# Kernel tuning notes

Measured on AMD Instinct MI355X. Metric: run time of the kernel, lower is better.

Reference implementation:

```python
import jax, jax.numpy as jnp
import numpy as np

H, KV, HD = 32, 4, 64
REP = H // KV
MAX_POS = 2048


def setup_inputs() -> dict:
    key = jax.random.key(0)
    ks = jax.random.split(key, 6)
    B, S, D = 2, 1024, 2048
    x = jax.random.normal(ks[0], (B, S, D), dtype=jnp.float32)
    wq = jax.random.normal(ks[1], (D, H * HD), dtype=jnp.float32) * 0.02
    wk = jax.random.normal(ks[2], (D, KV * HD), dtype=jnp.float32) * 0.02
    wv = jax.random.normal(ks[3], (D, KV * HD), dtype=jnp.float32) * 0.02
    wo = jax.random.normal(ks[4], (H * HD, D), dtype=jnp.float32) * 0.02
    # RoPE tables: [max_pos, head_dim//2]
    inv_freq = 1.0 / (10000.0 ** (np.arange(0, HD, 2, dtype=np.float32) / HD))
    angles = np.arange(MAX_POS, dtype=np.float32)[:, None] * inv_freq[None, :]
    cos = jnp.asarray(np.cos(angles), dtype=jnp.float32)
    sin = jnp.asarray(np.sin(angles), dtype=jnp.float32)
    # causal additive mask [S, S]
    row = jnp.arange(S)[:, None]
    col = jnp.arange(S)[None, :]
    mask = jnp.where(col <= row, 0.0, -1e9).astype(jnp.float32)
    return {"x": x, "wq": wq, "wk": wk, "wv": wv, "wo": wo,
            "cos": cos, "sin": sin, "mask": mask, "pos": 0}


def _rotate(t, c, s):
    # t: [B,S,Hx,HD]; c,s: [1,S,1,HD//2]
    half = t.shape[-1] // 2
    t1, t2 = t[..., :half], t[..., half:]
    return jnp.concatenate([t1 * c - t2 * s, t2 * c + t1 * s], axis=-1)


def reference(x, wq, wk, wv, wo, cos, sin, mask, pos):
    B, S, D = x.shape
    q = (x @ wq).reshape(B, S, H, HD)
    k = (x @ wk).reshape(B, S, KV, HD)
    v = (x @ wv).reshape(B, S, KV, HD)
    c = cos[pos:pos + S][None, :, None, :]
    s = sin[pos:pos + S][None, :, None, :]
    q = _rotate(q, c, s)
    k = _rotate(k, c, s)
    # prefill: cache[:, 0:S] == fresh k,v, kv_len == S
    # native GQA broadcast: group q heads by kv head instead of repeating k/v
    qg = q.reshape(B, S, KV, REP, HD)
    scores = jnp.einsum('bqkrd,bskd->bkrqs', qg, k) / jnp.sqrt(jnp.float32(HD))
    scores = scores + mask  # mask broadcasts over [B,KV,REP,S,S]
    attn = jax.nn.softmax(scores, axis=-1)
    out = jnp.einsum('bkrqs,bskd->bqkrd', attn, v).reshape(B, S, H * HD)
    return out @ wo
```

## Files before the change

kernel.cpp:

```cpp
#include <hip/hip_runtime.h>

#define B_ 2
#define S_ 1024
#define D_ 2048
#define H_ 32
#define KV_ 4
#define HD_ 64
#define NQKV 2560
#define KVB 64

typedef __attribute__((ext_vector_type(8))) short bf16x8;
typedef __attribute__((ext_vector_type(4))) float f32x4;
typedef __attribute__((ext_vector_type(16))) float f32x16;

__device__ __forceinline__ unsigned short f2bf(float f) {
  unsigned int u = __float_as_uint(f);
  u = (u + 0x7fffu + ((u >> 16) & 1u)) >> 16;
  return (unsigned short)u;
}
__device__ __forceinline__ unsigned int cvt_pk_bf16(float a, float b) {
  unsigned int r;
  asm("v_cvt_pk_bf16_f32 %0, %1, %2" : "=v"(r) : "v"(a), "v"(b));
  return r;
}
__device__ __forceinline__ float exp2f_fast(float x) {
  return __builtin_amdgcn_exp2f(x);
}

#define GLOAD_LDS(gp, lp) \
  __builtin_amdgcn_global_load_lds((const __attribute__((address_space(1))) void*)(gp), \
                                   (__attribute__((address_space(3))) void*)(lp), 16, 0, 0)

__global__ __launch_bounds__(256) void k_convert(const float* __restrict__ src,
                                                 unsigned short* __restrict__ dst, int n4) {
  int i = blockIdx.x * 256 + threadIdx.x;
  if (i >= n4) return;
  float4 v = ((const float4*)src)[i];
  ushort4 o;
  o.x = f2bf(v.x); o.y = f2bf(v.y); o.z = f2bf(v.z); o.w = f2bf(v.w);
  ((ushort4*)dst)[i] = o;
}

__global__ __launch_bounds__(256) void k_transpose4(const float* __restrict__ wq,
                                                    const float* __restrict__ wk,
                                                    const float* __restrict__ wv,
                                                    const float* __restrict__ wo,
                                                    unsigned short* __restrict__ wft,
                                                    unsigned short* __restrict__ wot) {
  __shared__ float tile[32][33];
  const int z = blockIdx.z;
  const float* src;
  unsigned short* dst;
  int N, roff;
  if (z == 0)      { src = wq; dst = wft; N = 2048; roff = 0; }
  else if (z == 1) { src = wk; dst = wft; N = 256;  roff = 2048; }
  else if (z == 2) { src = wv; dst = wft; N = 256;  roff = 2304; }
  else             { src = wo; dst = wot; N = 2048; roff = 0; }
  int n0 = blockIdx.x * 32, k0 = blockIdx.y * 32;
  if (n0 >= N) return;
  int tx = threadIdx.x & 31, ty = threadIdx.x >> 5;
  #pragma unroll
  for (int i = 0; i < 4; ++i)
    tile[ty + 8 * i][tx] = src[(size_t)(k0 + ty + 8 * i) * N + (n0 + tx)];
  __syncthreads();
  #pragma unroll
  for (int i = 0; i < 4; ++i)
    dst[(size_t)(roff + n0 + ty + 8 * i) * D_ + (k0 + tx)] = f2bf(tile[tx][ty + 8 * i]);
}

template <int BM, int BN, int MODE>
__global__ __launch_bounds__(256) void k_gemm(const unsigned short* __restrict__ A,
                                              const unsigned short* __restrict__ Bt,
                                              float* __restrict__ C,
                                              const float* __restrict__ cosT,
                                              const float* __restrict__ sinT,
                                              const int* __restrict__ posp,
                                              unsigned short* __restrict__ q_r,
                                              unsigned short* __restrict__ k_r,
                                              unsigned short* __restrict__ v_t,
                                              int M, int N, int K) {
  constexpr int MR = BM / 32;
  constexpr int NR = BN / 32;
  __shared__ alignas(16) unsigned short As[BM * 64];
  __shared__ alignas(16) unsigned short Bs[BN * 64];
  const int tid = threadIdx.x;
  const int wid = tid >> 6, lane = tid & 63;
  const int lo = lane & 15, hi = lane >> 4;
  const int m0 = blockIdx.y * BM, n0 = blockIdx.x * BN;
  const int wr = wid >> 1, wc = wid & 1;
  f32x4 acc[MR][NR] = {};

  const int nkt = K >> 6;
  for (int kt = 0; kt < nkt; ++kt) {
    __syncthreads();
    #pragma unroll
    for (int u = tid; u < BM * 8; u += 256) {
      int row = u >> 3, ch = u & 7, chs = ch ^ (row & 7);
      GLOAD_LDS(A + (size_t)(m0 + row) * K + kt * 64 + chs * 8, As + u * 8);
    }
    #pragma unroll
    for (int u = tid; u < BN * 8; u += 256) {
      int row = u >> 3, ch = u & 7, chs = ch ^ (row & 7);
      GLOAD_LDS(Bt + (size_t)(n0 + row) * K + kt * 64 + chs * 8, Bs + u * 8);
    }
    __syncthreads();
    #pragma unroll
    for (int ks = 0; ks < 2; ++ks) {
      const int chs = (ks * 4 + hi) ^ (lo & 7);
      bf16x8 a[MR], b[NR];
      #pragma unroll
      for (int m = 0; m < MR; ++m) {
        int row = wr * (BM / 2) + m * 16 + lo;
        a[m] = *(const bf16x8*)(As + row * 64 + chs * 8);
      }
      #pragma unroll
      for (int n = 0; n < NR; ++n) {
        int row = wc * (BN / 2) + n * 16 + lo;
        b[n] = *(const bf16x8*)(Bs + row * 64 + chs * 8);
      }
      #pragma unroll
      for (int m = 0; m < MR; ++m)
        #pragma unroll
        for (int n = 0; n < NR; ++n)
          acc[m][n] = __builtin_amdgcn_mfma_f32_16x16x32_bf16(a[m], b[n], acc[m][n], 0, 0, 0);
    }
  }

  if (MODE == 0) {
    const int cr = hi * 4;
    #pragma unroll
    for (int m = 0; m < MR; ++m)
      #pragma unroll
      for (int n = 0; n < NR; ++n) {
        int col = n0 + wc * (BN / 2) + n * 16 + lo;
        int rowb = m0 + wr * (BM / 2) + m * 16 + cr;
        #pragma unroll
        for (int r = 0; r < 4; ++r)
          C[(size_t)(rowb + r) * N + col] = acc[m][n][r];
      }
  } else {
    const int col0 = n0 + wc * (BN / 2);
    const int pos = posp[0];
    const float qsc = 0.125f * 1.44269504f;
    if (col0 < 2048) {
      const int h = col0 >> 6;
      #pragma unroll
      for (int m = 0; m < MR; ++m)
        #pragma unroll
        for (int r = 0; r < 4; ++r) {
          int row = m0 + wr * (BM / 2) + m * 16 + hi * 4 + r;
          int s = row & (S_ - 1), b = row >> 10;
          unsigned short* base = q_r + ((size_t)(b * H_ + h) * S_ + s) * HD_;
          #pragma unroll
          for (int np = 0; np < 2; ++np) {
            int i = np * 16 + lo;
            float t1 = acc[m][np][r], t2 = acc[m][np + 2][r];
            float c = cosT[(size_t)(pos + s) * 32 + i];
            float sn = sinT[(size_t)(pos + s) * 32 + i];
            base[i] = f2bf((t1 * c - t2 * sn) * qsc);
            base[i + 32] = f2bf((t2 * c + t1 * sn) * qsc);
          }
        }
    } else if (col0 < 2304) {
      const int g = (col0 - 2048) >> 6;
      #pragma unroll
      for (int m = 0; m < MR; ++m)
        #pragma unroll
        for (int r = 0; r < 4; ++r) {
          int row = m0 + wr * (BM / 2) + m * 16 + hi * 4 + r;
          int s = row & (S_ - 1), b = row >> 10;
          unsigned short* base = k_r + ((size_t)(b * KV_ + g) * S_ + s) * HD_;
          #pragma unroll
          for (int np = 0; np < 2; ++np) {
            int i = np * 16 + lo;
            float t1 = acc[m][np][r], t2 = acc[m][np + 2][r];
            float c = cosT[(size_t)(pos + s) * 32 + i];
            float sn = sinT[(size_t)(pos + s) * 32 + i];
            base[i] = f2bf(t1 * c - t2 * sn);
            base[i + 32] = f2bf(t2 * c + t1 * sn);
          }
        }
    } else {
      const int g = (col0 - 2304) >> 6;
      #pragma unroll
      for (int m = 0; m < MR; ++m) {
        int row0 = m0 + wr * (BM / 2) + m * 16 + hi * 4;
        int s0 = row0 & (S_ - 1), b = row0 >> 10;
        #pragma unroll
        for (int n = 0; n < NR; ++n) {
          int d = n * 16 + lo;
          ushort4 o;
          o.x = f2bf(acc[m][n][0]);
          o.y = f2bf(acc[m][n][1]);
          o.z = f2bf(acc[m][n][2]);
          o.w = f2bf(acc[m][n][3]);
          *(ushort4*)(v_t + ((size_t)(b * KV_ + g) * HD_ + d) * S_ + s0) = o;
        }
      }
    }
  }
}

__global__ __launch_bounds__(128) void k_attn(const unsigned short* __restrict__ qr,
                                              const unsigned short* __restrict__ kr,
                                              const unsigned short* __restrict__ vt,
                                              unsigned short* __restrict__ ao) {
  __shared__ alignas(16) unsigned short k_lds[2 * KVB * HD_];
  __shared__ alignas(16) unsigned short v_lds[2 * HD_ * KVB];
  const int tid = threadIdx.x;
  const int wid = tid >> 6, lane = tid & 63;
  const int l31 = lane & 31, hi5 = lane >> 5;
  const int bh = blockIdx.x;
  const int h = bh >> 1, b = bh & 1, g = h >> 3;
  const int qt = 15 - (int)blockIdx.y;
  const int nch = qt + 1;
  const int q_abs = qt * 64 + wid * 32 + l31;

  const unsigned short* qrow = qr + ((size_t)(b * H_ + h) * S_ + q_abs) * HD_;
  bf16x8 qf[4];
  #pragma unroll
  for (int ks = 0; ks < 4; ++ks)
    qf[ks] = *(const bf16x8*)(qrow + ks * 16 + hi5 * 8);

  const unsigned short* kbase = kr + (size_t)(b * KV_ + g) * S_ * HD_;
  const unsigned short* vbase = vt + (size_t)(b * KV_ + g) * HD_ * S_;

  const unsigned short* kg[4];
  const unsigned short* vg[4];
  int ldo[4];
  #pragma unroll
  for (int ii = 0; ii < 4; ++ii) {
    int uu = ii * 128 + tid;
    int r = uu >> 3, ch = uu & 7, chs = ch ^ (r & 7);
    kg[ii] = kbase + r * HD_ + chs * 8;
    vg[ii] = vbase + (size_t)r * S_ + chs * 8;
    ldo[ii] = uu * 8;
  }
  int chs8[4];
  #pragma unroll
  for (int ks = 0; ks < 4; ++ks) chs8[ks] = ((ks * 2 + hi5) ^ (l31 & 7)) * 8;
  const int krow = l31 * 64;

  f32x16 oacc[2] = {};
  float mrun = -1e30f, ls = 0.f;
  int buf = 0;

  auto stage = [&](int c, int bi) {
    #pragma unroll
    for (int ii = 0; ii < 4; ++ii)
      GLOAD_LDS(kg[ii] + (size_t)c * (KVB * HD_), k_lds + bi * 4096 + ldo[ii]);
    #pragma unroll
    for (int ii = 0; ii < 4; ++ii)
      GLOAD_LDS(vg[ii] + (size_t)c * KVB, v_lds + bi * 4096 + ldo[ii]);
  };

  stage(0, 0);
  __syncthreads();

  for (int c = 0; c < nch; ++c) {
    if (c + 1 < nch) stage(c + 1, buf ^ 1);
    const unsigned short* kl = k_lds + buf * 4096;
    const unsigned short* vl = v_lds + buf * 4096;
    const int j0 = c * KVB;

    f32x16 st[2] = {};
    __builtin_amdgcn_s_setprio(1);
    #pragma unroll
    for (int ks = 0; ks < 4; ++ks)
      #pragma unroll
      for (int jt = 0; jt < 2; ++jt) {
        bf16x8 kf = *(const bf16x8*)(kl + jt * 2048 + krow + chs8[ks]);
        st[jt] = __builtin_amdgcn_mfma_f32_32x32x16_bf16(kf, qf[ks], st[jt], 0, 0, 0);
      }
    __builtin_amdgcn_s_setprio(0);

    float pmax = -1e30f;
    if (c == nch - 1) {
      #pragma unroll
      for (int jt = 0; jt < 2; ++jt)
        #pragma unroll
        for (int r = 0; r < 16; ++r) {
          int j_abs = j0 + jt * 32 + (r & 3) + 8 * (r >> 2) + 4 * hi5;
          if (j_abs > q_abs) st[jt][r] = -1e30f;
          pmax = fmaxf(pmax, st[jt][r]);
        }
    } else {
      #pragma unroll
      for (int jt = 0; jt < 2; ++jt)
        #pragma unroll
        for (int r = 0; r < 16; ++r) pmax = fmaxf(pmax, st[jt][r]);
    }
    pmax = fmaxf(pmax, __shfl_xor(pmax, 32, 64));

    if (__any(pmax > mrun)) {
      float mn = fmaxf(mrun, pmax);
      float scale = exp2f_fast(mrun - mn);
      ls *= scale;
      #pragma unroll
      for (int dt = 0; dt < 2; ++dt)
        #pragma unroll
        for (int r = 0; r < 16; ++r) oacc[dt][r] *= scale;
      mrun = mn;
    }
    float ls0 = 0.f, ls1 = 0.f, ls2 = 0.f, ls3 = 0.f;
    #pragma unroll
    for (int jt = 0; jt < 2; ++jt)
      #pragma unroll
      for (int r = 0; r < 16; ++r) {
        float e = exp2f_fast(st[jt][r] - mrun);
        st[jt][r] = e;
        if ((r & 3) == 0) ls0 += e; else if ((r & 3) == 1) ls1 += e;
        else if ((r & 3) == 2) ls2 += e; else ls3 += e;
      }
    ls += (ls0 + ls1) + (ls2 + ls3);

    unsigned int pk[2][4][2];
    #pragma unroll
    for (int jt = 0; jt < 2; ++jt)
      #pragma unroll
      for (int qd = 0; qd < 4; ++qd) {
        pk[jt][qd][0] = cvt_pk_bf16(st[jt][qd * 4 + 0], st[jt][qd * 4 + 1]);
        pk[jt][qd][1] = cvt_pk_bf16(st[jt][qd * 4 + 2], st[jt][qd * 4 + 3]);
      }

    bf16x8 pf[4];
    #pragma unroll
    for (int jt = 0; jt < 2; ++jt) {
      unsigned int ex0a = hi5 ? pk[jt][0][0] : pk[jt][1][0];
      unsigned int ex0b = hi5 ? pk[jt][0][1] : pk[jt][1][1];
      unsigned int ex1a = hi5 ? pk[jt][2][0] : pk[jt][3][0];
      unsigned int ex1b = hi5 ? pk[jt][2][1] : pk[jt][3][1];
      unsigned int rA0 = (unsigned int)__shfl_xor((int)ex0a, 32, 64);
      unsigned int rA1 = (unsigned int)__shfl_xor((int)ex0b, 32, 64);
      unsigned int rB0 = (unsigned int)__shfl_xor((int)ex1a, 32, 64);
      unsigned int rB1 = (unsigned int)__shfl_xor((int)ex1b, 32, 64);
      union { unsigned int w[4]; bf16x8 v; } fe, fo;
      if (hi5) {
        fe.w[0] = rA0; fe.w[1] = rA1; fe.w[2] = pk[jt][1][0]; fe.w[3] = pk[jt][1][1];
        fo.w[0] = rB0; fo.w[1] = rB1; fo.w[2] = pk[jt][3][0]; fo.w[3] = pk[jt][3][1];
      } else {
        fe.w[0] = pk[jt][0][0]; fe.w[1] = pk[jt][0][1]; fe.w[2] = rA0; fe.w[3] = rA1;
        fo.w[0] = pk[jt][2][0]; fo.w[1] = pk[jt][2][1]; fo.w[2] = rB0; fo.w[3] = rB1;
      }
      pf[jt * 2 + 0] = fe.v;
      pf[jt * 2 + 1] = fo.v;
    }

    __builtin_amdgcn_s_setprio(1);
    #pragma unroll
    for (int ks = 0; ks < 4; ++ks)
      #pragma unroll
      for (int dt = 0; dt < 2; ++dt) {
        bf16x8 vf = *(const bf16x8*)(vl + dt * 2048 + krow + chs8[ks]);
        oacc[dt] = __builtin_amdgcn_mfma_f32_32x32x16_bf16(vf, pf[ks], oacc[dt], 0, 0, 0);
      }
    __builtin_amdgcn_s_setprio(0);

    __syncthreads();
    buf ^= 1;
  }

  float tot = ls + __shfl_xor(ls, 32, 64);
  float inv = 1.f / tot;
  unsigned short* orow = ao + (size_t)(b * S_ + q_abs) * (H_ * HD_) + h * HD_;
  #pragma unroll
  for (int dt = 0; dt < 2; ++dt)
    #pragma unroll
    for (int rg = 0; rg < 4; ++rg) {
      uint2 w;
      w.x = cvt_pk_bf16(oacc[dt][rg * 4 + 0] * inv, oacc[dt][rg * 4 + 1] * inv);
      w.y = cvt_pk_bf16(oacc[dt][rg * 4 + 2] * inv, oacc[dt][rg * 4 + 3] * inv);
      *(uint2*)(orow + dt * 32 + rg * 8 + hi5 * 4) = w;
    }
}

extern "C" void kernel_launch(void* const* d_in, const int* in_sizes, int n_in,
                              void* d_out, int out_size, void* d_ws, size_t ws_size,
                              hipStream_t stream) {
  const float* x    = (const float*)d_in[0];
  const float* wq   = (const float*)d_in[1];
  const float* wk   = (const float*)d_in[2];
  const float* wv   = (const float*)d_in[3];
  const float* wo   = (const float*)d_in[4];
  const float* cosT = (const float*)d_in[5];
  const float* sinT = (const float*)d_in[6];
  const int*   posp = (const int*)d_in[8];
  float* out = (float*)d_out;

  char* ws = (char*)d_ws;
  size_t off = 0;
  auto alloc = [&](size_t bytes) {
    char* p = ws + off;
    off += (bytes + 255) & ~(size_t)255;
    return p;
  };
  unsigned short* xb  = (unsigned short*)alloc((size_t)B_ * S_ * D_ * 2);
  unsigned short* wft = (unsigned short*)alloc((size_t)NQKV * D_ * 2);
  unsigned short* wot = (unsigned short*)alloc((size_t)D_ * D_ * 2);
  unsigned short* q_r = (unsigned short*)alloc((size_t)B_ * H_ * S_ * HD_ * 2);
  unsigned short* k_r = (unsigned short*)alloc((size_t)B_ * KV_ * S_ * HD_ * 2);
  unsigned short* v_t = (unsigned short*)alloc((size_t)B_ * KV_ * HD_ * S_ * 2);
  unsigned short* ao  = (unsigned short*)alloc((size_t)B_ * S_ * H_ * HD_ * 2);
  if (off > ws_size) return;

  k_convert<<<(B_ * S_ * D_ / 4 + 255) / 256, 256, 0, stream>>>(x, xb, B_ * S_ * D_ / 4);
  k_transpose4<<<dim3(D_ / 32, D_ / 32, 4), 256, 0, stream>>>(wq, wk, wv, wo, wft, wot);

  k_gemm<64, 128, 1><<<dim3(NQKV / 128, (B_ * S_) / 64), 256, 0, stream>>>(
      xb, wft, nullptr, cosT, sinT, posp, q_r, k_r, v_t, B_ * S_, NQKV, D_);

  k_attn<<<dim3(64, 16), 128, 0, stream>>>(q_r, k_r, v_t, ao);

  k_gemm<64, 128, 0><<<dim3(D_ / 128, (B_ * S_) / 64), 256, 0, stream>>>(
      ao, wot, out, nullptr, nullptr, nullptr, nullptr, nullptr, nullptr, B_ * S_, D_, D_);
}
```

Before: 110.4 us.

## Split-K both GEMMs with 128x128 tiles and separate reduce+RoPE kernels

Both projection GEMMs switch to 128x128 tiles with a 2-way split over K, writing fp32 partials to a workspace buffer. Separate kernels then sum the partials and apply RoPE, scaling, bf16 conversion and the V transpose, which were previously fused into the GEMM epilogue. The intent is to keep the grid filled while using larger tiles for more data reuse, and s_setprio is added around the MFMA block. The cost is extra fp32 partial traffic (tens of MB) and four additional kernel launches.

```diff
diff --git a/kernel.cpp b/kernel.cpp
--- a/kernel.cpp
+++ b/kernel.cpp
@@ -68,17 +68,11 @@
     dst[(size_t)(roff + n0 + ty + 8 * i) * D_ + (k0 + tx)] = f2bf(tile[tx][ty + 8 * i]);
 }
 
-template <int BM, int BN, int MODE>
-__global__ __launch_bounds__(256) void k_gemm(const unsigned short* __restrict__ A,
-                                              const unsigned short* __restrict__ Bt,
-                                              float* __restrict__ C,
-                                              const float* __restrict__ cosT,
-                                              const float* __restrict__ sinT,
-                                              const int* __restrict__ posp,
-                                              unsigned short* __restrict__ q_r,
-                                              unsigned short* __restrict__ k_r,
-                                              unsigned short* __restrict__ v_t,
-                                              int M, int N, int K) {
+template <int BM, int BN>
+__global__ __launch_bounds__(256) void k_gemm_sk(const unsigned short* __restrict__ A,
+                                                 const unsigned short* __restrict__ Bt,
+                                                 float* __restrict__ P,
+                                                 int M, int N, int K) {
   constexpr int MR = BM / 32;
   constexpr int NR = BN / 32;
   __shared__ alignas(16) unsigned short As[BM * 64];
@@ -87,21 +81,24 @@
   const int wid = tid >> 6, lane = tid & 63;
   const int lo = lane & 15, hi = lane >> 4;
   const int m0 = blockIdx.y * BM, n0 = blockIdx.x * BN;
+  const int kz = blockIdx.z;
+  const int KH = K >> 1;
+  const int kbase = kz * KH;
   const int wr = wid >> 1, wc = wid & 1;
   f32x4 acc[MR][NR] = {};
 
-  const int nkt = K >> 6;
+  const int nkt = KH >> 6;
   for (int kt = 0; kt < nkt; ++kt) {
     __syncthreads();
     #pragma unroll
     for (int u = tid; u < BM * 8; u += 256) {
       int row = u >> 3, ch = u & 7, chs = ch ^ (row & 7);
-      GLOAD_LDS(A + (size_t)(m0 + row) * K + kt * 64 + chs * 8, As + u * 8);
+      GLOAD_LDS(A + (size_t)(m0 + row) * K + kbase + kt * 64 + chs * 8, As + u * 8);
     }
     #pragma unroll
     for (int u = tid; u < BN * 8; u += 256) {
       int row = u >> 3, ch = u & 7, chs = ch ^ (row & 7);
-      GLOAD_LDS(Bt + (size_t)(n0 + row) * K + kt * 64 + chs * 8, Bs + u * 8);
+      GLOAD_LDS(Bt + (size_t)(n0 + row) * K + kbase + kt * 64 + chs * 8, Bs + u * 8);
     }
     __syncthreads();
     #pragma unroll
@@ -118,87 +115,99 @@
         int row = wc * (BN / 2) + n * 16 + lo;
         b[n] = *(const bf16x8*)(Bs + row * 64 + chs * 8);
       }
+      __builtin_amdgcn_s_setprio(1);
       #pragma unroll
       for (int m = 0; m < MR; ++m)
         #pragma unroll
         for (int n = 0; n < NR; ++n)
           acc[m][n] = __builtin_amdgcn_mfma_f32_16x16x32_bf16(a[m], b[n], acc[m][n], 0, 0, 0);
+      __builtin_amdgcn_s_setprio(0);
     }
   }
 
-  if (MODE == 0) {
-    const int cr = hi * 4;
-    #pragma unroll
-    for (int m = 0; m < MR; ++m)
-      #pragma unroll
-      for (int n = 0; n < NR; ++n) {
-        int col = n0 + wc * (BN / 2) + n * 16 + lo;
-        int rowb = m0 + wr * (BM / 2) + m * 16 + cr;
-        #pragma unroll
-        for (int r = 0; r < 4; ++r)
-          C[(size_t)(rowb + r) * N + col] = acc[m][n][r];
-      }
-  } else {
-    const int col0 = n0 + wc * (BN / 2);
-    const int pos = posp[0];
-    const float qsc = 0.125f * 1.44269504f;
-    if (col0 < 2048) {
-      const int h = col0 >> 6;
-      #pragma unroll
-      for (int m = 0; m < MR; ++m)
-        #pragma unroll
-        for (int r = 0; r < 4; ++r) {
-          int row = m0 + wr * (BM / 2) + m * 16 + hi * 4 + r;
-          int s = row & (S_ - 1), b = row >> 10;
-          unsigned short* base = q_r + ((size_t)(b * H_ + h) * S_ + s) * HD_;
-          #pragma unroll
-          for (int np = 0; np < 2; ++np) {
-            int i = np * 16 + lo;
-            float t1 = acc[m][np][r], t2 = acc[m][np + 2][r];
-            float c = cosT[(size_t)(pos + s) * 32 + i];
-            float sn = sinT[(size_t)(pos + s) * 32 + i];
-            base[i] = f2bf((t1 * c - t2 * sn) * qsc);
-            base[i + 32] = f2bf((t2 * c + t1 * sn) * qsc);
-          }
-        }
-    } else if (col0 < 2304) {
-      const int g = (col0 - 2048) >> 6;
-      #pragma unroll
-      for (int m = 0; m < MR; ++m)
-        #pragma unroll
-        for (int r = 0; r < 4; ++r) {
-          int row = m0 + wr * (BM / 2) + m * 16 + hi * 4 + r;
-          int s = row & (S_ - 1), b = row >> 10;
-          unsigned short* base = k_r + ((size_t)(b * KV_ + g) * S_ + s) * HD_;
-          #pragma unroll
-          for (int np = 0; np < 2; ++np) {
-            int i = np * 16 + lo;
-            float t1 = acc[m][np][r], t2 = acc[m][np + 2][r];
-            float c = cosT[(size_t)(pos + s) * 32 + i];
-            float sn = sinT[(size_t)(pos + s) * 32 + i];
-            base[i] = f2bf(t1 * c - t2 * sn);
-            base[i + 32] = f2bf(t2 * c + t1 * sn);
-          }
-        }
-    } else {
-      const int g = (col0 - 2304) >> 6;
-      #pragma unroll
-      for (int m = 0; m < MR; ++m) {
-        int row0 = m0 + wr * (BM / 2) + m * 16 + hi * 4;
-        int s0 = row0 & (S_ - 1), b = row0 >> 10;
-        #pragma unroll
-        for (int n = 0; n < NR; ++n) {
-          int d = n * 16 + lo;
-          ushort4 o;
-          o.x = f2bf(acc[m][n][0]);
-          o.y = f2bf(acc[m][n][1]);
-          o.z = f2bf(acc[m][n][2]);
-          o.w = f2bf(acc[m][n][3]);
-          *(ushort4*)(v_t + ((size_t)(b * KV_ + g) * HD_ + d) * S_ + s0) = o;
-        }
-      }
-    }
+  float* Pz = P + (size_t)kz * M * N;
+  const int cr = hi * 4;
+  #pragma unroll
+  for (int m = 0; m < MR; ++m)
+    #pragma unroll
+    for (int n = 0; n < NR; ++n) {
+      int col = n0 + wc * (BN / 2) + n * 16 + lo;
+      int rowb = m0 + wr * (BM / 2) + m * 16 + cr;
+      #pragma unroll
+      for (int r = 0; r < 4; ++r)
+        Pz[(size_t)(rowb + r) * N + col] = acc[m][n][r];
+    }
+}
+
+__global__ __launch_bounds__(256) void k_rope_q_red(const float* __restrict__ P,
+                                                    const float* __restrict__ cosT,
+                                                    const float* __restrict__ sinT,
+                                                    const int* __restrict__ posp,
+                                                    unsigned short* __restrict__ q_r) {
+  const size_t MN = (size_t)(B_ * S_) * NQKV;
+  int t = blockIdx.x * 256 + threadIdx.x;
+  int i = t & 31, h = (t >> 5) & 31, s = (t >> 10) & 1023, b = t >> 20;
+  int pos = posp[0];
+  const float qsc = 0.125f * 1.44269504f;
+  size_t idx = (size_t)(b * S_ + s) * NQKV + h * HD_ + i;
+  float q1 = P[idx] + P[idx + MN];
+  float q2 = P[idx + 32] + P[idx + 32 + MN];
+  float c = cosT[(size_t)(pos + s) * 32 + i], sn = sinT[(size_t)(pos + s) * 32 + i];
+  unsigned short* base = q_r + ((size_t)(b * H_ + h) * S_ + s) * HD_;
+  base[i] = f2bf((q1 * c - q2 * sn) * qsc);
+  base[i + 32] = f2bf((q2 * c + q1 * sn) * qsc);
+}
+
+__global__ __launch_bounds__(256) void k_rope_k_red(const float* __restrict__ P,
+                                                    const float* __restrict__ cosT,
+                                                    const float* __restrict__ sinT,
+                                                    const int* __restrict__ posp,
+                                                    unsigned short* __restrict__ k_r) {
+  const size_t MN = (size_t)(B_ * S_) * NQKV;
+  int t = blockIdx.x * 256 + threadIdx.x;
+  int i = t & 31, g = (t >> 5) & 3, s = (t >> 7) & 1023, b = t >> 17;
+  int pos = posp[0];
+  size_t idx = (size_t)(b * S_ + s) * NQKV + 2048 + g * HD_ + i;
+  float k1 = P[idx] + P[idx + MN];
+  float k2 = P[idx + 32] + P[idx + 32 + MN];
+  float c = cosT[(size_t)(pos + s) * 32 + i], sn = sinT[(size_t)(pos + s) * 32 + i];
+  unsigned short* base = k_r + ((size_t)(b * KV_ + g) * S_ + s) * HD_;
+  base[i] = f2bf(k1 * c - k2 * sn);
+  base[i + 32] = f2bf(k2 * c + k1 * sn);
+}
+
+__global__ __launch_bounds__(256) void k_vt_red(const float* __restrict__ P,
+                                                unsigned short* __restrict__ v_t) {
+  const size_t MN = (size_t)(B_ * S_) * NQKV;
+  __shared__ float tile[32][33];
+  int bg = blockIdx.z;
+  int b = bg >> 2, g = bg & 3;
+  int s0 = blockIdx.x * 32, d0 = blockIdx.y * 32;
+  int tx = threadIdx.x & 31, ty = threadIdx.x >> 5;
+  #pragma unroll
+  for (int i = 0; i < 4; ++i) {
+    int s = s0 + ty + 8 * i;
+    size_t idx = (size_t)(b * S_ + s) * NQKV + 2304 + g * HD_ + d0 + tx;
+    tile[ty + 8 * i][tx] = P[idx] + P[idx + MN];
   }
+  __syncthreads();
+  #pragma unroll
+  for (int i = 0; i < 4; ++i) {
+    int d = d0 + ty + 8 * i;
+    v_t[((size_t)bg * HD_ + d) * S_ + s0 + tx] = f2bf(tile[tx][ty + 8 * i]);
+  }
+}
+
+__global__ __launch_bounds__(256) void k_out_red(const float* __restrict__ P,
+                                                 float* __restrict__ out, int n4) {
+  const size_t MN = (size_t)(B_ * S_) * D_;
+  int i = blockIdx.x * 256 + threadIdx.x;
+  if (i >= n4) return;
+  float4 a = ((const float4*)P)[i];
+  float4 b = ((const float4*)(P + MN))[i];
+  float4 o;
+  o.x = a.x + b.x; o.y = a.y + b.y; o.z = a.z + b.z; o.w = a.w + b.w;
+  ((float4*)out)[i] = o;
 }
 
 __global__ __launch_bounds__(128) void k_attn(const unsigned short* __restrict__ qr,
@@ -401,16 +410,21 @@
   unsigned short* k_r = (unsigned short*)alloc((size_t)B_ * KV_ * S_ * HD_ * 2);
   unsigned short* v_t = (unsigned short*)alloc((size_t)B_ * KV_ * HD_ * S_ * 2);
   unsigned short* ao  = (unsigned short*)alloc((size_t)B_ * S_ * H_ * HD_ * 2);
+  float*          P   = (float*)alloc((size_t)2 * B_ * S_ * NQKV * 4);
   if (off > ws_size) return;
 
   k_convert<<<(B_ * S_ * D_ / 4 + 255) / 256, 256, 0, stream>>>(x, xb, B_ * S_ * D_ / 4);
   k_transpose4<<<dim3(D_ / 32, D_ / 32, 4), 256, 0, stream>>>(wq, wk, wv, wo, wft, wot);
 
-  k_gemm<64, 128, 1><<<dim3(NQKV / 128, (B_ * S_) / 64), 256, 0, stream>>>(
-      xb, wft, nullptr, cosT, sinT, posp, q_r, k_r, v_t, B_ * S_, NQKV, D_);
+  k_gemm_sk<128, 128><<<dim3(NQKV / 128, (B_ * S_) / 128, 2), 256, 0, stream>>>(
+      xb, wft, P, B_ * S_, NQKV, D_);
+  k_rope_q_red<<<(B_ * S_ * H_ * 32) / 256, 256, 0, stream>>>(P, cosT, sinT, posp, q_r);
+  k_rope_k_red<<<(B_ * S_ * KV_ * 32) / 256, 256, 0, stream>>>(P, cosT, sinT, posp, k_r);
+  k_vt_red<<<dim3(S_ / 32, HD_ / 32, B_ * KV_), 256, 0, stream>>>(P, v_t);
 
   k_attn<<<dim3(64, 16), 128, 0, stream>>>(q_r, k_r, v_t, ao);
 
-  k_gemm<64, 128, 0><<<dim3(D_ / 128, (B_ * S_) / 64), 256, 0, stream>>>(
-      ao, wot, out, nullptr, nullptr, nullptr, nullptr, nullptr, nullptr, B_ * S_, D_, D_);
-}
+  k_gemm_sk<128, 128><<<dim3(D_ / 128, (B_ * S_) / 128, 2), 256, 0, stream>>>(
+      ao, wot, P, B_ * S_, D_, D_);
+  k_out_red<<<(B_ * S_ * D_ / 4 + 255) / 256, 256, 0, stream>>>(P, out, B_ * S_ * D_ / 4);
+}
```

Measured after the change: 124.7 us, median of 2. 12.9% more time.
